# Optimization experiments

Measured on AMD Instinct MI355X. Metric: run time of the kernel, lower is better.

The kernel has to match this reference:

```python
import jax, jax.numpy as jnp
import numpy as np


def setup_inputs() -> dict:
    key = jax.random.key(0)
    ks = jax.random.split(key, 8)
    B, C, H, W = 4, 256, 64, 64
    QP = 32  # query_planes = inplanes // 8
    x = jax.random.normal(ks[0], (B, C, H, W), dtype=jnp.float32)
    Wq = jax.random.normal(ks[1], (QP, C), dtype=jnp.float32) * (1.0 / np.sqrt(C))
    bq = jax.random.normal(ks[2], (QP,), dtype=jnp.float32) * 0.01
    Wk = jax.random.normal(ks[3], (QP, C), dtype=jnp.float32) * (1.0 / np.sqrt(C))
    bk = jax.random.normal(ks[4], (QP,), dtype=jnp.float32) * 0.01
    Wv = jax.random.normal(ks[5], (C, C), dtype=jnp.float32) * (1.0 / np.sqrt(C))
    bv = jax.random.normal(ks[6], (C,), dtype=jnp.float32) * 0.01
    gamma = jax.random.normal(ks[7], (), dtype=jnp.float32)
    return {"x": x, "Wq": Wq, "bq": bq, "Wk": Wk, "bk": bk,
            "Wv": Wv, "bv": bv, "gamma": gamma}


def reference(x, Wq, bq, Wk, bk, Wv, bv, gamma):
    B, C, H, W = x.shape
    N = H * W
    flat = x.reshape(B, C, N)                              # [B, C, N]
    # 1x1 Conv1d == pointwise linear over channel dim
    q = jnp.einsum('qc,bcn->bnq', Wq, flat) + bq[None, None, :]   # [B, N, QP] (already permuted)
    k = jnp.einsum('qc,bcn->bqn', Wk, flat) + bk[None, :, None]   # [B, QP, N]
    v = jnp.einsum('oc,bcn->bon', Wv, flat) + bv[None, :, None]   # [B, C, N]
    # scores[b, i, j] = <q_i, k_j>, NO 1/sqrt(d) scaling (as in source)
    scores = jnp.einsum('biq,bqj->bij', q, k)              # [B, N, N]
    # unusual softmax axis: dim=1 == over query positions i, per column j
    attn = jax.nn.softmax(scores, axis=1)                  # [B, N, N]
    out_attn = jnp.einsum('bcn,bnj->bcj', v, attn)         # [B, C, N]
    out_attn = out_attn.reshape(B, C, H, W)
    return gamma * out_attn + x
```

## Files before the change

kernel.cpp:

```cpp
#include <hip/hip_runtime.h>
#include <hip/hip_bf16.h>
#include <math.h>


#define NBATCH 4
#define CDIM   256
#define NSEQ   4096
#define QPDIM  32
#define LOG2E  1.44269504088896340736f

typedef _Float16 half8_t  __attribute__((ext_vector_type(8)));
typedef _Float16 half2_t  __attribute__((ext_vector_type(2)));
typedef float    floatx4  __attribute__((ext_vector_type(4)));
typedef float    floatx16 __attribute__((ext_vector_type(16)));

union H8 { half8_t h8; half2_t h2[4]; int i32[4]; };

__device__ inline half2_t pack_f16(float a, float b) {
    return __builtin_bit_cast(half2_t, __builtin_amdgcn_cvt_pkrtz(a, b));
}

__global__ __launch_bounds__(256) void wprep_kernel(
    const float* __restrict__ Wv, const float* __restrict__ Wq,
    const float* __restrict__ Wk, _Float16* __restrict__ wH)
{
    const int idx = blockIdx.x * 256 + threadIdx.x;
    const int e = idx * 8;
    const int r = e >> 8, c = e & 255;
    const float* src;
    float scale = 1.0f;
    if (r < 256)      src = Wv + (size_t)r * 256 + c;
    else if (r < 288) { src = Wq + (size_t)(r - 256) * 256 + c; scale = LOG2E; }
    else              src = Wk + (size_t)(r - 288) * 256 + c;
    float4 f0 = ((const float4*)src)[0];
    float4 f1 = ((const float4*)src)[1];
    half8_t h;
    h[0] = (_Float16)(f0.x * scale); h[1] = (_Float16)(f0.y * scale);
    h[2] = (_Float16)(f0.z * scale); h[3] = (_Float16)(f0.w * scale);
    h[4] = (_Float16)(f1.x * scale); h[5] = (_Float16)(f1.y * scale);
    h[6] = (_Float16)(f1.z * scale); h[7] = (_Float16)(f1.w * scale);
    *(half8_t*)(wH + (size_t)r * 256 + c) = h;
}

__global__ __launch_bounds__(256, 2) void qkv_kernel(
    const float* __restrict__ x, const _Float16* __restrict__ wH,
    const float* __restrict__ bq, const float* __restrict__ bk,
    const float* __restrict__ bv,
    _Float16* __restrict__ qH, _Float16* __restrict__ kH,
    _Float16* __restrict__ vHT)
{
    __shared__ _Float16 xT[32][264];

    const int blk  = blockIdx.x;
    const int slot = blk & 7;
    const int b    = slot >> 1;
    const int n0   = (((blk >> 3) << 1) | (slot & 1)) << 5;
    const int t    = threadIdx.x;
    const int w    = t >> 6;
    const int lane = t & 63;
    const int quad = lane >> 4;
    const int col  = lane & 15;

    {
        const int crow0 = t >> 3;
        const int npart = t & 7;
        #pragma unroll
        for (int pass = 0; pass < 8; ++pass) {
            const int c = pass * 32 + crow0;
            float4 f = *(const float4*)(
                x + ((size_t)(b * CDIM + c)) * NSEQ + n0 + npart * 4);
            xT[npart * 4 + 0][c] = (_Float16)f.x;
            xT[npart * 4 + 1][c] = (_Float16)f.y;
            xT[npart * 4 + 2][c] = (_Float16)f.z;
            xT[npart * 4 + 3][c] = (_Float16)f.w;
        }
    }
    __syncthreads();

    const int r0 = w * 80;
    floatx4 acc[5][2];
    #pragma unroll
    for (int mt = 0; mt < 5; ++mt)
        #pragma unroll
        for (int nt = 0; nt < 2; ++nt)
            acc[mt][nt] = (floatx4){0.f, 0.f, 0.f, 0.f};

    #pragma unroll
    for (int ks = 0; ks < 8; ++ks) {
        half8_t bf[2];
        #pragma unroll
        for (int nt = 0; nt < 2; ++nt)
            bf[nt] = *(const half8_t*)&xT[nt * 16 + col][ks * 32 + quad * 8];
        #pragma unroll
        for (int mt = 0; mt < 5; ++mt) {
            half8_t a = *(const half8_t*)(
                wH + (size_t)(r0 + mt * 16 + col) * 256 + ks * 32 + quad * 8);
            #pragma unroll
            for (int nt = 0; nt < 2; ++nt)
                acc[mt][nt] = __builtin_amdgcn_mfma_f32_16x16x32_f16(
                    a, bf[nt], acc[mt][nt], 0, 0, 0);
        }
    }

    #pragma unroll
    for (int mt = 0; mt < 5; ++mt) {
        const int gbase = r0 + mt * 16;
        const float* bp; int rl; float bscale = 1.0f;
        if (gbase < 256)      { bp = bv; rl = gbase; }
        else if (gbase < 288) { bp = bq; rl = gbase - 256; bscale = LOG2E; }
        else                  { bp = bk; rl = gbase - 288; }
        #pragma unroll
        for (int reg = 0; reg < 4; ++reg) {
            const int rr = rl + quad * 4 + reg;
            const float bias = bp[rr] * bscale;
            #pragma unroll
            for (int nt = 0; nt < 2; ++nt) {
                const int n = n0 + nt * 16 + col;
                const float val = acc[mt][nt][reg] + bias;
                if (gbase < 256)
                    vHT[((size_t)(b * CDIM + rr)) * NSEQ + n] = (_Float16)val;
                else if (gbase < 288)
                    qH[((size_t)(b * NSEQ + n)) * QPDIM + rr] = (_Float16)val;
                else
                    kH[((size_t)(b * NSEQ + n)) * QPDIM + rr] = (_Float16)val;
            }
        }
    }
}

__global__ __launch_bounds__(256, 4) void mpass_kernel(
    const _Float16* __restrict__ qH, const _Float16* __restrict__ kH,
    float* __restrict__ ms4)
{
    __shared__ float wmax[4][32];

    const int blk  = blockIdx.x;
    const int slot = blk & 7;
    const int b    = slot >> 1;
    const int idx  = ((blk >> 3) << 1) | (slot & 1);
    const int jblk = idx & 63;
    const int iq   = idx >> 6;
    const int t    = threadIdx.x;
    const int w    = t >> 6;
    const int lane = t & 63;
    const int l5   = lane >> 5;
    const int lj   = lane & 31;
    const int jt   = w & 1, ih = w >> 1;

    const _Float16* qg = qH + (size_t)b * NSEQ * QPDIM;
    const int j = jblk * 64 + jt * 32 + lj;
    const half8_t kb0 = *(const half8_t*)(
        kH + ((size_t)(b * NSEQ + j)) * QPDIM + l5 * 8);
    const half8_t kb1 = *(const half8_t*)(
        kH + ((size_t)(b * NSEQ + j)) * QPDIM + 16 + l5 * 8);

    float mx = -1e30f;
    const int ibase = iq * 1024 + ih * 512;
    for (int cc = 0; cc < 16; ++cc) {
        const _Float16* qp = qg + (size_t)(ibase + cc * 32 + lj) * QPDIM + l5 * 8;
        half8_t qa0 = *(const half8_t*)qp;
        half8_t qa1 = *(const half8_t*)(qp + 16);
        floatx16 S = __builtin_amdgcn_mfma_f32_32x32x16_f16(
            qa0, kb0, (floatx16){0.f}, 0, 0, 0);
        S = __builtin_amdgcn_mfma_f32_32x32x16_f16(qa1, kb1, S, 0, 0, 0);
        float t0 = fmaxf(fmaxf(S[0],  S[1]),  S[2]);
        float t1 = fmaxf(fmaxf(S[3],  S[4]),  S[5]);
        float t2 = fmaxf(fmaxf(S[6],  S[7]),  S[8]);
        float t3 = fmaxf(fmaxf(S[9],  S[10]), S[11]);
        float t4 = fmaxf(fmaxf(S[12], S[13]), S[14]);
        mx = fmaxf(mx, fmaxf(fmaxf(fmaxf(t0, t1), fmaxf(t2, t3)),
                             fmaxf(t4, S[15])));
    }
    mx = fmaxf(mx, __shfl_xor(mx, 32));
    if (lane < 32) wmax[w][lane] = mx;
    __syncthreads();
    if (t < 64) {
        const int jt3 = t >> 5, c = t & 31;
        ms4[(size_t)iq * (NBATCH * NSEQ) + (size_t)b * NSEQ
            + jblk * 64 + jt3 * 32 + c] = fmaxf(wmax[jt3][c], wmax[jt3 + 2][c]);
    }
}

__global__ __launch_bounds__(512, 1) void attn_kernel(
    const _Float16* __restrict__ qH, const _Float16* __restrict__ kH,
    const _Float16* __restrict__ vHT, const float* __restrict__ ms4,
    const float* __restrict__ x, const float* __restrict__ gamma,
    float* __restrict__ out)
{
    __shared__ _Float16 vbuf[2][32768];
    __shared__ float lred[2][4][32];

    const int blk  = blockIdx.x;
    const int slot = blk & 7;
    const int b    = slot >> 1;
    const int jblk = ((blk >> 3) << 1) | (slot & 1);
    const int j0   = jblk << 6;
    const int t    = threadIdx.x;
    const int w    = t >> 6;
    const int lane = t & 63;
    const int l5   = lane >> 5;
    const int lj   = lane & 31;
    const int jh   = w & 1;
    const int ih   = w >> 1;

    const _Float16* qg = qH + (size_t)b * NSEQ * QPDIM;
    const _Float16* vg = vHT + (size_t)b * CDIM * NSEQ;

    const int jme = j0 + jh * 32 + lj;
    const half8_t kb0 = *(const half8_t*)(
        kH + ((size_t)(b * NSEQ + jme)) * QPDIM + l5 * 8);
    const half8_t kb1 = *(const half8_t*)(
        kH + ((size_t)(b * NSEQ + jme)) * QPDIM + 16 + l5 * 8);
    const float* msb = ms4 + (size_t)b * NSEQ + jme;
    const float mfix = fmaxf(
        fmaxf(msb[0], msb[NBATCH * NSEQ]),
        fmaxf(msb[2 * NBATCH * NSEQ], msb[3 * NBATCH * NSEQ]));
    floatx16 Sinit;
    #pragma unroll
    for (int r = 0; r < 16; ++r) Sinit[r] = -mfix;

    floatx16 acc[8];
    #pragma unroll
    for (int ct = 0; ct < 8; ++ct) acc[ct] = (floatx16){0.f};
    float lp = 0.0f;

    #define DMA_V(i0_, buf_)                                                   \
        {                                                                      \
            _Pragma("unroll")                                                  \
            for (int g = 0; g < 8; ++g) {                                      \
                const int uu = w * 512 + g * 64 + lane;                        \
                const int cl = uu >> 4;                                        \
                const int ck = (uu & 15) ^ (cl & 7);                           \
                const _Float16* src =                                          \
                    vg + (size_t)cl * NSEQ + (i0_) + ck * 8;                   \
                __builtin_amdgcn_global_load_lds(                              \
                    (const __attribute__((address_space(1))) void*)src,        \
                    (__attribute__((address_space(3))) void*)                  \
                        (&vbuf[buf_][(w * 512 + g * 64) * 8]),                 \
                    16, 0, 0);                                                 \
            }                                                                  \
        }

    DMA_V(0, 0);
    const _Float16* qb = qg + (size_t)(ih * 32 + lj) * QPDIM + l5 * 8;
    half8_t qa0 = *(const half8_t*)(qb);
    half8_t qa1 = *(const half8_t*)(qb + 16);

    int cur = 0;
    for (int i0 = 0; i0 < NSEQ; i0 += 128) {
        __syncthreads();
        if (i0 + 128 < NSEQ) DMA_V(i0 + 128, cur ^ 1);

        floatx16 S = __builtin_amdgcn_mfma_f32_32x32x16_f16(
            qa0, kb0, Sinit, 0, 0, 0);
        S = __builtin_amdgcn_mfma_f32_32x32x16_f16(qa1, kb1, S, 0, 0, 0);

        if (i0 + 128 < NSEQ) {
            qa0 = *(const half8_t*)(qb + (size_t)(i0 + 128) * QPDIM);
            qa1 = *(const half8_t*)(qb + (size_t)(i0 + 128) * QPDIM + 16);
        }

        H8 lo, hi;
        float ls = 0.0f;
        #pragma unroll
        for (int p = 0; p < 4; ++p) {
            float pa = __builtin_amdgcn_exp2f(S[2 * p]);
            float pb = __builtin_amdgcn_exp2f(S[2 * p + 1]);
            ls += pa + pb;
            lo.h2[p] = pack_f16(pa, pb);
        }
        #pragma unroll
        for (int p = 0; p < 4; ++p) {
            float pa = __builtin_amdgcn_exp2f(S[8 + 2 * p]);
            float pb = __builtin_amdgcn_exp2f(S[8 + 2 * p + 1]);
            ls += pa + pb;
            hi.h2[p] = pack_f16(pa, pb);
        }
        lp += ls;

        H8 P0, P1;
#if __has_builtin(__builtin_amdgcn_permlane32_swap)
        {
            auto r0p = __builtin_amdgcn_permlane32_swap(
                (unsigned)lo.i32[0], (unsigned)lo.i32[2], false, false);
            P0.i32[0] = (int)r0p[0]; P0.i32[2] = (int)r0p[1];
            auto r1p = __builtin_amdgcn_permlane32_swap(
                (unsigned)lo.i32[1], (unsigned)lo.i32[3], false, false);
            P0.i32[1] = (int)r1p[0]; P0.i32[3] = (int)r1p[1];
            auto r2p = __builtin_amdgcn_permlane32_swap(
                (unsigned)hi.i32[0], (unsigned)hi.i32[2], false, false);
            P1.i32[0] = (int)r2p[0]; P1.i32[2] = (int)r2p[1];
            auto r3p = __builtin_amdgcn_permlane32_swap(
                (unsigned)hi.i32[1], (unsigned)hi.i32[3], false, false);
            P1.i32[1] = (int)r3p[0]; P1.i32[3] = (int)r3p[1];
        }
#else
        {
            H8 shl, shh;
            #pragma unroll
            for (int r = 0; r < 4; ++r) {
                shl.i32[r] = __shfl_xor(lo.i32[r], 32);
                shh.i32[r] = __shfl_xor(hi.i32[r], 32);
            }
            const bool high = (l5 != 0);
            P0.i32[0] = high ? shl.i32[2] : lo.i32[0];
            P0.i32[1] = high ? shl.i32[3] : lo.i32[1];
            P0.i32[2] = high ? lo.i32[2]  : shl.i32[0];
            P0.i32[3] = high ? lo.i32[3]  : shl.i32[1];
            P1.i32[0] = high ? shh.i32[2] : hi.i32[0];
            P1.i32[1] = high ? shh.i32[3] : hi.i32[1];
            P1.i32[2] = high ? hi.i32[2]  : shh.i32[0];
            P1.i32[3] = high ? hi.i32[3]  : shh.i32[1];
        }
#endif

        __builtin_amdgcn_s_setprio(1);
        #pragma unroll
        for (int ct = 0; ct < 8; ++ct) {
            const int cl = ct * 32 + lj;
            const int ic0 = (ih * 4 + 0 + l5) ^ (cl & 7);
            const int ic1 = (ih * 4 + 2 + l5) ^ (cl & 7);
            half8_t va0 = *(const half8_t*)&vbuf[cur][(cl * 16 + ic0) * 8];
            half8_t va1 = *(const half8_t*)&vbuf[cur][(cl * 16 + ic1) * 8];
            acc[ct] = __builtin_amdgcn_mfma_f32_32x32x16_f16(
                va0, P0.h8, acc[ct], 0, 0, 0);
            acc[ct] = __builtin_amdgcn_mfma_f32_32x32x16_f16(
                va1, P1.h8, acc[ct], 0, 0, 0);
        }
        __builtin_amdgcn_s_setprio(0);

        cur ^= 1;
    }

    lp += __shfl_xor(lp, 32);
    if (lane < 32) lred[jh][ih][lane] = lp;
    __syncthreads();

    float* fred = (float*)vbuf;
    const int rA = jh * 2 + (ih >> 1);
    if (ih & 1) {
        float* rg = fred + rA * 8192;
        #pragma unroll
        for (int ct = 0; ct < 8; ++ct)
            #pragma unroll
            for (int reg = 0; reg < 16; ++reg) {
                const int crow = (reg & 3) + 8 * (reg >> 2) + 4 * l5;
                rg[(ct * 32 + crow) * 32 + lj] = acc[ct][reg];
            }
    }
    __syncthreads();
    if (!(ih & 1)) {
        float* rg = fred + rA * 8192;
        #pragma unroll
        for (int ct = 0; ct < 8; ++ct)
            #pragma unroll
            for (int reg = 0; reg < 16; ++reg) {
                const int crow = (reg & 3) + 8 * (reg >> 2) + 4 * l5;
                acc[ct][reg] += rg[(ct * 32 + crow) * 32 + lj];
            }
    }
    __syncthreads();
    if (ih == 0) {
        float* rg = fred + (jh * 2 + 0) * 8192;
        #pragma unroll
        for (int ct = 4; ct < 8; ++ct)
            #pragma unroll
            for (int reg = 0; reg < 16; ++reg) {
                const int crow = (reg & 3) + 8 * (reg >> 2) + 4 * l5;
                rg[(ct * 32 + crow) * 32 + lj] = acc[ct][reg];
            }
    } else if (ih == 2) {
        float* rg = fred + (jh * 2 + 1) * 8192;
        #pragma unroll
        for (int ct = 0; ct < 4; ++ct)
            #pragma unroll
            for (int reg = 0; reg < 16; ++reg) {
                const int crow = (reg & 3) + 8 * (reg >> 2) + 4 * l5;
                rg[(ct * 32 + crow) * 32 + lj] = acc[ct][reg];
            }
    }
    __syncthreads();
    if (ih == 0) {
        const float lsum = lred[jh][0][lj] + lred[jh][1][lj]
                         + lred[jh][2][lj] + lred[jh][3][lj];
        const float rv = gamma[0] / lsum;
        float* rg = fred + (jh * 2 + 1) * 8192;
        #pragma unroll
        for (int ct = 0; ct < 4; ++ct) {
            #pragma unroll
            for (int reg = 0; reg < 16; ++reg) {
                const int crow = (reg & 3) + 8 * (reg >> 2) + 4 * l5;
                const int c_ = ct * 32 + crow;
                const size_t off = ((size_t)(b * CDIM + c_)) * NSEQ + jme;
                const float sum =
                    acc[ct][reg] + rg[(ct * 32 + crow) * 32 + lj];
                out[off] = sum * rv + x[off];
            }
        }
    } else if (ih == 2) {
        const float lsum = lred[jh][0][lj] + lred[jh][1][lj]
                         + lred[jh][2][lj] + lred[jh][3][lj];
        const float rv = gamma[0] / lsum;
        float* rg = fred + (jh * 2 + 0) * 8192;
        #pragma unroll
        for (int ct = 4; ct < 8; ++ct) {
            #pragma unroll
            for (int reg = 0; reg < 16; ++reg) {
                const int crow = (reg & 3) + 8 * (reg >> 2) + 4 * l5;
                const int c_ = ct * 32 + crow;
                const size_t off = ((size_t)(b * CDIM + c_)) * NSEQ + jme;
                const float sum =
                    acc[ct][reg] + rg[(ct * 32 + crow) * 32 + lj];
                out[off] = sum * rv + x[off];
            }
        }
    }
}

extern "C" void kernel_launch(void* const* d_in, const int* in_sizes, int n_in,
                              void* d_out, int out_size, void* d_ws, size_t ws_size,
                              hipStream_t stream) {
    const float* x     = (const float*)d_in[0];
    const float* Wq    = (const float*)d_in[1];
    const float* bq    = (const float*)d_in[2];
    const float* Wk    = (const float*)d_in[3];
    const float* bk    = (const float*)d_in[4];
    const float* Wv    = (const float*)d_in[5];
    const float* bv    = (const float*)d_in[6];
    const float* gamma = (const float*)d_in[7];
    float* out = (float*)d_out;

    _Float16* w16 = (_Float16*)d_ws;
    _Float16* qH  = w16;
    _Float16* kH  = qH + (size_t)NBATCH * NSEQ * QPDIM;
    _Float16* vHT = kH + (size_t)NBATCH * NSEQ * QPDIM;
    _Float16* wH  = vHT + (size_t)NBATCH * CDIM * NSEQ;
    float*    ms4 = (float*)(wH + (size_t)320 * 256);

    wprep_kernel<<<40, 256, 0, stream>>>(Wv, Wq, Wk, wH);
    qkv_kernel<<<512, 256, 0, stream>>>(x, wH, bq, bk, bv, qH, kH, vHT);
    mpass_kernel<<<1024, 256, 0, stream>>>(qH, kH, ms4);
    attn_kernel<<<256, 512, 0, stream>>>(qH, kH, vHT, ms4, x, gamma, out);
}
```

Baseline: 162.9 us.

## Software-pipeline QK softmax of next tile with PV MFMAs of current tile

Restructures the main loop into a two-stage software pipeline, unrolled by two with fixed buffer indices. The QK^T MFMA and exp2 softmax for the next 128-row tile are computed before the PV MFMAs of the current tile, so exp/pack work can interleave with the matrix ops. Keeping two P tiles live raises register pressure, which could lower occupancy or cause spills.

```diff
diff --git a/kernel.cpp b/kernel.cpp
--- a/kernel.cpp
+++ b/kernel.cpp
@@ -18,6 +18,71 @@
 
 __device__ inline half2_t pack_f16(float a, float b) {
     return __builtin_bit_cast(half2_t, __builtin_amdgcn_cvt_pkrtz(a, b));
+}
+
+__device__ inline void transformP(const H8& lo, const H8& hi,
+                                  H8& P0, H8& P1, const int l5) {
+#if __has_builtin(__builtin_amdgcn_permlane32_swap)
+    {
+        auto r0p = __builtin_amdgcn_permlane32_swap(
+            (unsigned)lo.i32[0], (unsigned)lo.i32[2], false, false);
+        P0.i32[0] = (int)r0p[0]; P0.i32[2] = (int)r0p[1];
+        auto r1p = __builtin_amdgcn_permlane32_swap(
+            (unsigned)lo.i32[1], (unsigned)lo.i32[3], false, false);
+        P0.i32[1] = (int)r1p[0]; P0.i32[3] = (int)r1p[1];
+        auto r2p = __builtin_amdgcn_permlane32_swap(
+            (unsigned)hi.i32[0], (unsigned)hi.i32[2], false, false);
+        P1.i32[0] = (int)r2p[0]; P1.i32[2] = (int)r2p[1];
+        auto r3p = __builtin_amdgcn_permlane32_swap(
+            (unsigned)hi.i32[1], (unsigned)hi.i32[3], false, false);
+        P1.i32[1] = (int)r3p[0]; P1.i32[3] = (int)r3p[1];
+    }
+#else
+    {
+        H8 shl, shh;
+        #pragma unroll
+        for (int r = 0; r < 4; ++r) {
+            shl.i32[r] = __shfl_xor(lo.i32[r], 32);
+            shh.i32[r] = __shfl_xor(hi.i32[r], 32);
+        }
+        const bool high = (l5 != 0);
+        P0.i32[0] = high ? shl.i32[2] : lo.i32[0];
+        P0.i32[1] = high ? shl.i32[3] : lo.i32[1];
+        P0.i32[2] = high ? lo.i32[2]  : shl.i32[0];
+        P0.i32[3] = high ? lo.i32[3]  : shl.i32[1];
+        P1.i32[0] = high ? shh.i32[2] : hi.i32[0];
+        P1.i32[1] = high ? shh.i32[3] : hi.i32[1];
+        P1.i32[2] = high ? hi.i32[2]  : shh.i32[0];
+        P1.i32[3] = high ? hi.i32[3]  : shh.i32[1];
+    }
+#endif
+}
+
+__device__ inline void qk_softmax(half8_t qa0, half8_t qa1,
+                                  half8_t kb0, half8_t kb1,
+                                  const floatx16& Sinit, const int l5,
+                                  H8& P0, H8& P1, float& lp) {
+    floatx16 S = __builtin_amdgcn_mfma_f32_32x32x16_f16(
+        qa0, kb0, Sinit, 0, 0, 0);
+    S = __builtin_amdgcn_mfma_f32_32x32x16_f16(qa1, kb1, S, 0, 0, 0);
+    H8 lo, hi;
+    float ls = 0.0f;
+    #pragma unroll
+    for (int p = 0; p < 4; ++p) {
+        float pa = __builtin_amdgcn_exp2f(S[2 * p]);
+        float pb = __builtin_amdgcn_exp2f(S[2 * p + 1]);
+        ls += pa + pb;
+        lo.h2[p] = pack_f16(pa, pb);
+    }
+    #pragma unroll
+    for (int p = 0; p < 4; ++p) {
+        float pa = __builtin_amdgcn_exp2f(S[8 + 2 * p]);
+        float pb = __builtin_amdgcn_exp2f(S[8 + 2 * p + 1]);
+        ls += pa + pb;
+        hi.h2[p] = pack_f16(pa, pb);
+    }
+    lp += ls;
+    transformP(lo, hi, P0, P1, l5);
 }
 
 __global__ __launch_bounds__(256) void wprep_kernel(
@@ -241,95 +306,56 @@
             }                                                                  \
         }
 
+    #define PV_BLOCK(BUF_, Pa_, Pb_)                                           \
+        {                                                                      \
+            __builtin_amdgcn_s_setprio(1);                                     \
+            _Pragma("unroll")                                                  \
+            for (int ct = 0; ct < 8; ++ct) {                                   \
+                const int cl = ct * 32 + lj;                                   \
+                const int ic0 = (ih * 4 + 0 + l5) ^ (cl & 7);                  \
+                const int ic1 = (ih * 4 + 2 + l5) ^ (cl & 7);                  \
+                half8_t va0 =                                                  \
+                    *(const half8_t*)&vbuf[BUF_][(cl * 16 + ic0) * 8];         \
+                half8_t va1 =                                                  \
+                    *(const half8_t*)&vbuf[BUF_][(cl * 16 + ic1) * 8];         \
+                acc[ct] = __builtin_amdgcn_mfma_f32_32x32x16_f16(              \
+                    va0, Pa_.h8, acc[ct], 0, 0, 0);                            \
+                acc[ct] = __builtin_amdgcn_mfma_f32_32x32x16_f16(              \
+                    va1, Pb_.h8, acc[ct], 0, 0, 0);                            \
+            }                                                                  \
+            __builtin_amdgcn_s_setprio(0);                                     \
+        }
+
     DMA_V(0, 0);
     const _Float16* qb = qg + (size_t)(ih * 32 + lj) * QPDIM + l5 * 8;
-    half8_t qa0 = *(const half8_t*)(qb);
-    half8_t qa1 = *(const half8_t*)(qb + 16);
-
-    int cur = 0;
-    for (int i0 = 0; i0 < NSEQ; i0 += 128) {
+
+    half8_t qaA0 = *(const half8_t*)(qb);
+    half8_t qaA1 = *(const half8_t*)(qb + 16);
+    half8_t qaB0 = *(const half8_t*)(qb + (size_t)128 * QPDIM);
+    half8_t qaB1 = *(const half8_t*)(qb + (size_t)128 * QPDIM + 16);
+    H8 PA0, PA1, PB0, PB1;
+    qk_softmax(qaA0, qaA1, kb0, kb1, Sinit, l5, PA0, PA1, lp);
+
+    for (int i0 = 0; i0 < NSEQ; i0 += 256) {
         __syncthreads();
-        if (i0 + 128 < NSEQ) DMA_V(i0 + 128, cur ^ 1);
-
-        floatx16 S = __builtin_amdgcn_mfma_f32_32x32x16_f16(
-            qa0, kb0, Sinit, 0, 0, 0);
-        S = __builtin_amdgcn_mfma_f32_32x32x16_f16(qa1, kb1, S, 0, 0, 0);
-
-        if (i0 + 128 < NSEQ) {
-            qa0 = *(const half8_t*)(qb + (size_t)(i0 + 128) * QPDIM);
-            qa1 = *(const half8_t*)(qb + (size_t)(i0 + 128) * QPDIM + 16);
-        }
-
-        H8 lo, hi;
-        float ls = 0.0f;
-        #pragma unroll
-        for (int p = 0; p < 4; ++p) {
-            float pa = __builtin_amdgcn_exp2f(S[2 * p]);
-            float pb = __builtin_amdgcn_exp2f(S[2 * p + 1]);
-            ls += pa + pb;
-            lo.h2[p] = pack_f16(pa, pb);
-        }
-        #pragma unroll
-        for (int p = 0; p < 4; ++p) {
-            float pa = __builtin_amdgcn_exp2f(S[8 + 2 * p]);
-            float pb = __builtin_amdgcn_exp2f(S[8 + 2 * p + 1]);
-            ls += pa + pb;
-            hi.h2[p] = pack_f16(pa, pb);
-        }
-        lp += ls;
-
-        H8 P0, P1;
-#if __has_builtin(__builtin_amdgcn_permlane32_swap)
-        {
-            auto r0p = __builtin_amdgcn_permlane32_swap(
-                (unsigned)lo.i32[0], (unsigned)lo.i32[2], false, false);
-            P0.i32[0] = (int)r0p[0]; P0.i32[2] = (int)r0p[1];
-            auto r1p = __builtin_amdgcn_permlane32_swap(
-                (unsigned)lo.i32[1], (unsigned)lo.i32[3], false, false);
-            P0.i32[1] = (int)r1p[0]; P0.i32[3] = (int)r1p[1];
-            auto r2p = __builtin_amdgcn_permlane32_swap(
-                (unsigned)hi.i32[0], (unsigned)hi.i32[2], false, false);
-            P1.i32[0] = (int)r2p[0]; P1.i32[2] = (int)r2p[1];
-            auto r3p = __builtin_amdgcn_permlane32_swap(
-                (unsigned)hi.i32[1], (unsigned)hi.i32[3], false, false);
-            P1.i32[1] = (int)r3p[0]; P1.i32[3] = (int)r3p[1];
-        }
-#else
-        {
-            H8 shl, shh;
-            #pragma unroll
-            for (int r = 0; r < 4; ++r) {
-                shl.i32[r] = __shfl_xor(lo.i32[r], 32);
-                shh.i32[r] = __shfl_xor(hi.i32[r], 32);
-            }
-            const bool high = (l5 != 0);
-            P0.i32[0] = high ? shl.i32[2] : lo.i32[0];
-            P0.i32[1] = high ? shl.i32[3] : lo.i32[1];
-            P0.i32[2] = high ? lo.i32[2]  : shl.i32[0];
-            P0.i32[3] = high ? lo.i32[3]  : shl.i32[1];
-            P1.i32[0] = high ? shh.i32[2] : hi.i32[0];
-            P1.i32[1] = high ? shh.i32[3] : hi.i32[1];
-            P1.i32[2] = high ? hi.i32[2]  : shh.i32[0];
-            P1.i32[3] = high ? hi.i32[3]  : shh.i32[1];
-        }
-#endif
-
-        __builtin_amdgcn_s_setprio(1);
-        #pragma unroll
-        for (int ct = 0; ct < 8; ++ct) {
-            const int cl = ct * 32 + lj;
-            const int ic0 = (ih * 4 + 0 + l5) ^ (cl & 7);
-            const int ic1 = (ih * 4 + 2 + l5) ^ (cl & 7);
-            half8_t va0 = *(const half8_t*)&vbuf[cur][(cl * 16 + ic0) * 8];
-            half8_t va1 = *(const half8_t*)&vbuf[cur][(cl * 16 + ic1) * 8];
-            acc[ct] = __builtin_amdgcn_mfma_f32_32x32x16_f16(
-                va0, P0.h8, acc[ct], 0, 0, 0);
-            acc[ct] = __builtin_amdgcn_mfma_f32_32x32x16_f16(
-                va1, P1.h8, acc[ct], 0, 0, 0);
-        }
-        __builtin_amdgcn_s_setprio(0);
-
-        cur ^= 1;
+        DMA_V(i0 + 128, 1);
+        if (i0 + 256 < NSEQ) {
+            qaA0 = *(const half8_t*)(qb + (size_t)(i0 + 256) * QPDIM);
+            qaA1 = *(const half8_t*)(qb + (size_t)(i0 + 256) * QPDIM + 16);
+        }
+        qk_softmax(qaB0, qaB1, kb0, kb1, Sinit, l5, PB0, PB1, lp);
+        PV_BLOCK(0, PA0, PA1);
+
+        __syncthreads();
+        if (i0 + 256 < NSEQ) {
+            DMA_V(i0 + 256, 0);
+            if (i0 + 384 < NSEQ) {
+                qaB0 = *(const half8_t*)(qb + (size_t)(i0 + 384) * QPDIM);
+                qaB1 = *(const half8_t*)(qb + (size_t)(i0 + 384) * QPDIM + 16);
+            }
+            qk_softmax(qaA0, qaA1, kb0, kb1, Sinit, l5, PA0, PA1, lp);
+        }
+        PV_BLOCK(1, PB0, PB1);
     }
 
     lp += __shfl_xor(lp, 32);
```

Result: slower. 193.3 us (+18.6%).
